# Kernel tuning notes

Measured on AMD Instinct MI355X. Metric: run time of the kernel, lower is better.

Reference implementation:

```python
import jax, jax.numpy as jnp
import numpy as np

# ---- constants from the module ----
E_L, E_e, E_i = -65.0, 0.0, -80.0
V_th, V_reset, V_floor = -50.0, -65.0, -200.0
dt = 0.25
T_STEPS = 4000
DECAY_AMPA = float(np.exp(-dt / 2.0))   # tau_ampa = 2.0
DECAY_GABA = float(np.exp(-dt / 9.0))   # tau_gaba = 9.0
C_M_E, G_L_E = 1.0, 1.0 / 20.0          # tau_m_E = 20
C_M_I, G_L_I = 0.5, 0.5 / 5.0           # tau_m_I = 5
REF_E = 12                               # round(3.0/0.25)
REF_I = 6                                # round(1.5/0.25)
CM_BACK = 80.0
SLOPE = 1.0                              # biophysical surrogate slope

@jax.custom_vjp
def spike(u):
    # Heaviside forward, fast-sigmoid surrogate backward (SurrogateSpike)
    return (u >= 0).astype(u.dtype)

def _spike_fwd(u):
    return (u >= 0).astype(u.dtype), u

def _spike_bwd(u, g):
    return (g * SLOPE / (1.0 + SLOPE * jnp.abs(u)) ** 2,)

spike.defvjp(_spike_fwd, _spike_bwd)

def _scale_grad(x, scale):
    # forward identity, gradient scaled by `scale`
    return x * scale + jax.lax.stop_gradient(x) * (1.0 - scale)

def lif_step(v, I_total, ref, C_m, g_L, ref_steps):
    dv = (dt / C_m) * (-g_L * (v - E_L) + I_total)
    dv = _scale_grad(dv, 1.0 / CM_BACK)
    v = jnp.maximum(v + dv, V_floor)
    ref = jnp.maximum(ref - 1, 0)
    can_spike = ref == 0
    s = spike(v - V_th) * can_spike.astype(v.dtype)
    spiked_or_ref = (s > 0) | ~can_spike
    v = jnp.where(spiked_or_ref, V_reset, v)
    ref = jnp.where(s > 0, ref_steps, ref)
    return v, s, ref

def setup_inputs() -> dict:
    key = jax.random.key(0)
    ks = jax.random.split(key, 6)
    T, B, N_IN, N_E, N_I, N_OUT = T_STEPS, 64, 64, 256, 64, 10

    def init_w(k, shape, mean, std):
        # init_weight: N(mean,std) clamped >=0, fan-in normalized
        w = jnp.maximum(jax.random.normal(k, shape, jnp.float32) * std + mean, 0.0)
        return w / shape[0]

    return {
        "input_spikes": (jax.random.uniform(ks[0], (T, B, N_IN)) < 0.02).astype(jnp.float32),
        "W_ff0": init_w(ks[1], (N_IN, N_E), 5.1, 3.8),
        "W_ff1": init_w(ks[2], (N_E, N_OUT), 5.1, 3.8),
        "W_ee": init_w(ks[3], (N_E, N_E), 0.0, 0.0),
        "W_ei": init_w(ks[4], (N_E, N_I), 1.0, 0.5),
        "W_ie": init_w(ks[5], (N_I, N_E), 3.0, 1.5),
    }

def reference(input_spikes, W_ff0, W_ff1, W_ee, W_ei, W_ie):
    # Dale's law: feedforward weights clamped >= 0 in forward
    W0 = jnp.maximum(W_ff0, 0.0)
    W1 = jnp.maximum(W_ff1, 0.0)
    B = input_spikes.shape[1]
    N_E, N_I, N_OUT = W0.shape[1], W_ei.shape[1], W1.shape[1]
    f32 = input_spikes.dtype

    z = lambda n: jnp.zeros((B, n), f32)
    vl = lambda n: jnp.full((B, n), E_L, f32)
    zr = lambda n: jnp.zeros((B, n), jnp.int32)

    carry0 = (vl(N_E), zr(N_E), z(N_E), z(N_E), z(N_E),   # E pop: v, ref, g_ampa, g_gaba, spikes
              vl(N_I), zr(N_I), z(N_I), z(N_I),           # I pop: v, ref, g_ampa, spikes
              vl(N_OUT), zr(N_OUT), z(N_OUT),             # out pop: v, ref, g_ampa
              z(N_OUT))                                    # output spike accumulator

    def step(c, s_in):
        v_e, r_e, ge_e, gi_e, s_e, v_i, r_i, ge_i, s_i, v_o, r_o, g_o, acc = c
        # exp_synapse: spike kicks first, then decay
        ge_e = (ge_e + s_in @ W0 + s_e @ W_ee) * DECAY_AMPA
        gi_e = (gi_e + s_i @ W_ie) * DECAY_GABA
        ge_i = (ge_i + s_e @ W_ei) * DECAY_AMPA
        # E neurons: COBA with excitation + inhibition
        v_e, s_e, r_e = lif_step(v_e, ge_e * (E_e - v_e) + gi_e * (E_i - v_e), r_e, C_M_E, G_L_E, REF_E)
        # I neurons: COBA excitation only
        v_i, s_i, r_i = lif_step(v_i, ge_i * (E_e - v_i), r_i, C_M_I, G_L_I, REF_I)
        # output layer driven by fresh E spikes
        g_o = (g_o + s_e @ W1) * DECAY_AMPA
        v_o, s_o, r_o = lif_step(v_o, g_o * (E_e - v_o), r_o, C_M_E, G_L_E, REF_E)
        acc = acc + s_o
        return (v_e, r_e, ge_e, gi_e, s_e, v_i, r_i, ge_i, s_i, v_o, r_o, g_o, acc), None

    cT, _ = jax.lax.scan(step, carry0, input_spikes)
    return cT[-1]  # [B, N_OUT] output spike counts over T_steps
```

## Files before the change

### kernel.cpp

```cpp
#include <hip/hip_runtime.h>
#include <math.h>

#pragma clang fp contract(off)

#define BB 64
#define N_IN 64
#define N_E 256
#define N_I 64
#define N_OUT 10

__device__ inline unsigned long long rfl64(unsigned long long x) {
  unsigned int lo = __builtin_amdgcn_readfirstlane((unsigned int)x);
  unsigned int hi = __builtin_amdgcn_readfirstlane((unsigned int)(x >> 32));
  return (((unsigned long long)hi) << 32) | (unsigned long long)lo;
}

__global__ __launch_bounds__(256, 1) void ping_kernel(
    const float* __restrict__ g_in,
    const float* __restrict__ g_W0,
    const float* __restrict__ g_W1,
    const float* __restrict__ g_Wee,
    const float* __restrict__ g_Wei,
    const float* __restrict__ g_Wie,
    float* __restrict__ g_out,
    int T, float dA, float dG)
{
  const int tid  = threadIdx.x;
  const int lane = tid & 63;
  const int wav  = tid >> 6;
  const int b    = blockIdx.x;
  const int col  = (lane < N_OUT) ? lane : 0;
  const int colO = 64 + col;

  __shared__ float sWie[N_I * N_E];
  __shared__ float sWeiO[N_E * 80];
  __shared__ float sZeroRow[256];
  __shared__ float sP[2][4][64];
  __shared__ float sKo[2][4][16];
  __shared__ __align__(16) unsigned sTag[2][4];
  __shared__ unsigned long long sME[2][4];
  __shared__ int sWee;

  {
    const float4* s0 = (const float4*)g_Wie; float4* d0 = (float4*)sWie;
    for (int k = tid; k < (N_I * N_E) / 4; k += 256) d0[k] = s0[k];
    {
      int j = tid;
      float* row = &sWeiO[j * 80];
      for (int c = 0; c < 64; ++c) row[c] = g_Wei[j * N_I + c];
      for (int o = 0; o < N_OUT; ++o) row[64 + o] = fmaxf(g_W1[j * N_OUT + o], 0.f);
      for (int c = 74; c < 80; ++c) row[c] = 0.f;
    }
  }
  sZeroRow[tid] = 0.f;
  if (tid < 4) { sME[0][tid] = 0ull; sME[1][tid] = 0ull; }
  if (tid < 8) sTag[tid >> 2][tid & 3] = 0u;
  if (tid == 0) sWee = 0;
  {
    bool any = false;
    const float4* p = (const float4*)g_Wee;
    for (int k = tid; k < (N_E * N_E) / 4; k += 256) {
      float4 x = p[k];
      any |= (x.x != 0.f) | (x.y != 0.f) | (x.z != 0.f) | (x.w != 0.f);
    }
    if (__ballot(any) != 0ull && lane == 0) sWee = 1;
  }
  __syncthreads();
  const int wee = sWee;

  float vE = -65.f, ge = 0.f, gi = 0.f; int rE = 0;
  float vI = -65.f, gI = 0.f; int rI = 0;
  float vO = -65.f, gO = 0.f, accO = 0.f; int rO = 0;

  unsigned long long mE = 0ull;
  unsigned long long mI = 0ull;

  float cur = g_in[b * N_IN + lane];
  float n1  = g_in[((T > 1 ? 1 : 0) * BB + b) * N_IN + lane];

  unsigned long long mInC = __ballot(cur != 0.f);
  unsigned long long aRemC = 0ull;
  bool vaC[4] = {false, false, false, false};
  float fwC[4];
  if (mInC) {
    unsigned long long a = mInC;
    int ja[4];
#pragma unroll
    for (int k = 0; k < 4; ++k) {
      vaC[k] = (a != 0ull); ja[k] = vaC[k] ? (__ffsll(a) - 1) : 0; a &= (a - 1ull);
    }
    aRemC = a;
#pragma unroll
    for (int k = 0; k < 4; ++k) fwC[k] = g_W0[ja[k] * N_E + tid];
  }

  const int base64 = wav * 64;

  if (!wee) {
    for (int t = 0; t < T; ++t) {
      const int slot = t & 1;
      const int tp = (t + 2 < T) ? (t + 2) : (T - 1);
      float n2 = g_in[(tp * BB + b) * N_IN + lane];

      float pEI = 0.f, kow = 0.f;
      {
        unsigned long long e = mE;
        while (e) {
          const float* qb[4];
#pragma unroll
          for (int k = 0; k < 4; ++k) {
            bool v = (e != 0ull); int j = v ? (__ffsll(e) - 1) : 0; e &= (e - 1ull);
            qb[k] = v ? &sWeiO[(base64 + j) * 80] : sZeroRow;
          }
          float fq[4], fr[4];
#pragma unroll
          for (int k = 0; k < 4; ++k) { fq[k] = qb[k][lane]; fr[k] = qb[k][colO]; }
#pragma unroll
          for (int k = 0; k < 4; ++k) pEI += fq[k];
#pragma unroll
          for (int k = 0; k < 4; ++k) kow += fr[k];
        }
      }

      sP[slot][wav][lane] = pEI;
      if (lane < 16) sKo[slot][wav][lane] = kow;
      asm volatile("s_waitcnt lgkmcnt(0)" ::: "memory");
      if (lane == 0) *((volatile unsigned*)&sTag[slot][wav]) = (unsigned)(t + 1);

      float kie = 0.f;
      {
        unsigned long long c = mI;
        while (c) {
          const float* pb[8];
#pragma unroll
          for (int k = 0; k < 8; ++k) {
            bool v = (c != 0ull); int j = v ? (__ffsll(c) - 1) : 0; c &= (c - 1ull);
            pb[k] = v ? &sWie[j * N_E] : sZeroRow;
          }
          float fI[8];
#pragma unroll
          for (int k = 0; k < 8; ++k) fI[k] = pb[k][tid];
#pragma unroll
          for (int k = 0; k < 8; ++k) kie += fI[k];
        }
      }

      float kin = 0.f;
      if (mInC) {
#pragma unroll
        for (int k = 0; k < 4; ++k) kin += vaC[k] ? fmaxf(fwC[k], 0.f) : 0.f;
        while (aRemC) {
          int j = __ffsll(aRemC) - 1; aRemC &= (aRemC - 1ull);
          kin += fmaxf(g_W0[j * N_E + tid], 0.f);
        }
      }

      ge = (ge + kin) * dA;
      gi = (gi + kie) * dG;
      {
        float t2 = ge * (0.f - vE);
        float t3 = gi * (-80.f - vE);
        float Itot = t2 + t3;
        float dv = 0.25f * ((-0.05f) * (vE - (-65.f)) + Itot);
        dv = dv * 0.0125f + dv * 0.9875f;
        vE = fmaxf(vE + dv, -200.f);
        rE = rE - 1; if (rE < 0) rE = 0;
        bool can = (rE == 0);
        bool sE = ((vE - (-50.f)) >= 0.f) && can;
        vE = (sE || !can) ? -65.f : vE;
        rE = sE ? 12 : rE;
        mE = __ballot(sE);
      }

      mInC = __ballot(n1 != 0.f);
      aRemC = 0ull;
      vaC[0] = vaC[1] = vaC[2] = vaC[3] = false;
      if (mInC) {
        unsigned long long a = mInC;
        int ja[4];
#pragma unroll
        for (int k = 0; k < 4; ++k) {
          vaC[k] = (a != 0ull); ja[k] = vaC[k] ? (__ffsll(a) - 1) : 0; a &= (a - 1ull);
        }
        aRemC = a;
#pragma unroll
        for (int k = 0; k < 4; ++k) fwC[k] = g_W0[ja[k] * N_E + tid];
      }

      {
        const unsigned want = (unsigned)(t + 1);
        const unsigned long long want2 = (((unsigned long long)want) << 32) | want;
        volatile unsigned long long* vt = (volatile unsigned long long*)&sTag[slot][0];
        while (true) {
          unsigned long long a0 = vt[0], a1 = vt[1];
          if (((a0 ^ want2) | (a1 ^ want2)) == 0ull) break;
        }
        asm volatile("" ::: "memory");
      }

      float p0 = sP[slot][0][lane], p1 = sP[slot][1][lane];
      float p2 = sP[slot][2][lane], p3 = sP[slot][3][lane];
      float k0 = sKo[slot][0][col], k1 = sKo[slot][1][col];
      float k2 = sKo[slot][2][col], k3 = sKo[slot][3][col];

      {
        float p = ((p0 + p1) + p2) + p3;
        gI = (gI + p) * dA;
        float Ii = gI * (0.f - vI);
        float dvi = 0.5f * ((-0.1f) * (vI - (-65.f)) + Ii);
        dvi = dvi * 0.0125f + dvi * 0.9875f;
        vI = fmaxf(vI + dvi, -200.f);
        rI = rI - 1; if (rI < 0) rI = 0;
        bool canI = (rI == 0);
        bool sI = ((vI - (-50.f)) >= 0.f) && canI;
        vI = (sI || !canI) ? -65.f : vI;
        rI = sI ? 6 : rI;
        mI = __ballot(sI);
      }

      {
        float ko = ((k0 + k1) + k2) + k3;
        gO = (gO + ko) * dA;
        float Io = gO * (0.f - vO);
        float dvo = 0.25f * ((-0.05f) * (vO - (-65.f)) + Io);
        dvo = dvo * 0.0125f + dvo * 0.9875f;
        vO = fmaxf(vO + dvo, -200.f);
        rO = rO - 1; if (rO < 0) rO = 0;
        bool canO = (rO == 0);
        bool sO = ((vO - (-50.f)) >= 0.f) && canO;
        vO = (sO || !canO) ? -65.f : vO;
        rO = sO ? 12 : rO;
        accO += sO ? 1.f : 0.f;
      }

      cur = n1; n1 = n2;
    }
  } else {
    unsigned long long we0 = 0ull, we1 = 0ull, we2 = 0ull, we3 = 0ull;
    for (int t = 0; t < T; ++t) {
      const int slot = t & 1;
      const int tp = (t + 2 < T) ? (t + 2) : (T - 1);
      float n2 = g_in[(tp * BB + b) * N_IN + lane];

      float pEI = 0.f, kow = 0.f;
      {
        unsigned long long e = mE;
        while (e) {
          const float* qb[4];
#pragma unroll
          for (int k = 0; k < 4; ++k) {
            bool v = (e != 0ull); int j = v ? (__ffsll(e) - 1) : 0; e &= (e - 1ull);
            qb[k] = v ? &sWeiO[(base64 + j) * 80] : sZeroRow;
          }
          float fq[4], fr[4];
#pragma unroll
          for (int k = 0; k < 4; ++k) { fq[k] = qb[k][lane]; fr[k] = qb[k][colO]; }
#pragma unroll
          for (int k = 0; k < 4; ++k) pEI += fq[k];
#pragma unroll
          for (int k = 0; k < 4; ++k) kow += fr[k];
        }
      }
      sP[slot][wav][lane] = pEI;
      if (lane < 16) sKo[slot][wav][lane] = kow;
      asm volatile("s_waitcnt lgkmcnt(0)" ::: "memory");
      if (lane == 0) *((volatile unsigned*)&sTag[slot][wav]) = (unsigned)(t + 1);

      float kie = 0.f;
      {
        unsigned long long c = mI;
        while (c) {
          const float* pb[8];
#pragma unroll
          for (int k = 0; k < 8; ++k) {
            bool v = (c != 0ull); int j = v ? (__ffsll(c) - 1) : 0; c &= (c - 1ull);
            pb[k] = v ? &sWie[j * N_E] : sZeroRow;
          }
          float fI[8];
#pragma unroll
          for (int k = 0; k < 8; ++k) fI[k] = pb[k][tid];
#pragma unroll
          for (int k = 0; k < 8; ++k) kie += fI[k];
        }
      }

      float kin = 0.f;
      if (mInC) {
#pragma unroll
        for (int k = 0; k < 4; ++k) kin += vaC[k] ? fmaxf(fwC[k], 0.f) : 0.f;
        while (aRemC) {
          int j = __ffsll(aRemC) - 1; aRemC &= (aRemC - 1ull);
          kin += fmaxf(g_W0[j * N_E + tid], 0.f);
        }
      }

      float kee = 0.f;
      {
        unsigned long long m0 = we0, m1 = we1, m2 = we2, m3 = we3;
        while (m0 | m1 | m2 | m3) {
          bool h0 = (m0 != 0ull), h1 = (m1 != 0ull), h2 = (m2 != 0ull), h3 = (m3 != 0ull);
          int idx = 0;
          if (h0)      { idx = __ffsll(m0) - 1;       m0 &= (m0 - 1ull); }
          else if (h1) { idx = 64 + __ffsll(m1) - 1;  m1 &= (m1 - 1ull); }
          else if (h2) { idx = 128 + __ffsll(m2) - 1; m2 &= (m2 - 1ull); }
          else if (h3) { idx = 192 + __ffsll(m3) - 1; m3 &= (m3 - 1ull); }
          kee += g_Wee[idx * N_E + tid];
        }
      }

      ge = ((ge + kin) + kee) * dA;
      gi = (gi + kie) * dG;
      {
        float t2 = ge * (0.f - vE);
        float t3 = gi * (-80.f - vE);
        float Itot = t2 + t3;
        float dv = 0.25f * ((-0.05f) * (vE - (-65.f)) + Itot);
        dv = dv * 0.0125f + dv * 0.9875f;
        vE = fmaxf(vE + dv, -200.f);
        rE = rE - 1; if (rE < 0) rE = 0;
        bool can = (rE == 0);
        bool sE = ((vE - (-50.f)) >= 0.f) && can;
        vE = (sE || !can) ? -65.f : vE;
        rE = sE ? 12 : rE;
        unsigned long long fresh = __ballot(sE);
        if (lane == 0) sME[slot][wav] = fresh;
        mE = fresh;
      }

      mInC = __ballot(n1 != 0.f);
      aRemC = 0ull;
      vaC[0] = vaC[1] = vaC[2] = vaC[3] = false;
      if (mInC) {
        unsigned long long a = mInC;
        int ja[4];
#pragma unroll
        for (int k = 0; k < 4; ++k) {
          vaC[k] = (a != 0ull); ja[k] = vaC[k] ? (__ffsll(a) - 1) : 0; a &= (a - 1ull);
        }
        aRemC = a;
#pragma unroll
        for (int k = 0; k < 4; ++k) fwC[k] = g_W0[ja[k] * N_E + tid];
      }

      {
        const unsigned want = (unsigned)(t + 1);
        const unsigned long long want2 = (((unsigned long long)want) << 32) | want;
        volatile unsigned long long* vt = (volatile unsigned long long*)&sTag[slot][0];
        while (true) {
          unsigned long long a0 = vt[0], a1 = vt[1];
          if (((a0 ^ want2) | (a1 ^ want2)) == 0ull) break;
        }
        asm volatile("" ::: "memory");
      }

      float p0 = sP[slot][0][lane], p1 = sP[slot][1][lane];
      float p2 = sP[slot][2][lane], p3 = sP[slot][3][lane];
      float k0 = sKo[slot][0][col], k1 = sKo[slot][1][col];
      float k2 = sKo[slot][2][col], k3 = sKo[slot][3][col];

      {
        float p = ((p0 + p1) + p2) + p3;
        gI = (gI + p) * dA;
        float Ii = gI * (0.f - vI);
        float dvi = 0.5f * ((-0.1f) * (vI - (-65.f)) + Ii);
        dvi = dvi * 0.0125f + dvi * 0.9875f;
        vI = fmaxf(vI + dvi, -200.f);
        rI = rI - 1; if (rI < 0) rI = 0;
        bool canI = (rI == 0);
        bool sI = ((vI - (-50.f)) >= 0.f) && canI;
        vI = (sI || !canI) ? -65.f : vI;
        rI = sI ? 6 : rI;
        mI = __ballot(sI);
      }

      {
        float ko = ((k0 + k1) + k2) + k3;
        gO = (gO + ko) * dA;
        float Io = gO * (0.f - vO);
        float dvo = 0.25f * ((-0.05f) * (vO - (-65.f)) + Io);
        dvo = dvo * 0.0125f + dvo * 0.9875f;
        vO = fmaxf(vO + dvo, -200.f);
        rO = rO - 1; if (rO < 0) rO = 0;
        bool canO = (rO == 0);
        bool sO = ((vO - (-50.f)) >= 0.f) && canO;
        vO = (sO || !canO) ? -65.f : vO;
        rO = sO ? 12 : rO;
        accO += sO ? 1.f : 0.f;
      }

      __syncthreads();
      we0 = rfl64(sME[slot][0]); we1 = rfl64(sME[slot][1]);
      we2 = rfl64(sME[slot][2]); we3 = rfl64(sME[slot][3]);

      cur = n1; n1 = n2;
    }
  }

  {
    float kd = 0.f;
    unsigned long long e = mE;
    while (e) {
      const float* rb[4];
#pragma unroll
      for (int k = 0; k < 4; ++k) {
        bool v = (e != 0ull); int j = v ? (__ffsll(e) - 1) : 0; e &= (e - 1ull);
        rb[k] = v ? &sWeiO[(base64 + j) * 80] : sZeroRow;
      }
      float fr[4];
#pragma unroll
      for (int k = 0; k < 4; ++k) fr[k] = rb[k][colO];
#pragma unroll
      for (int k = 0; k < 4; ++k) kd += fr[k];
    }
    __syncthreads();
    sP[0][wav][lane] = kd;
    __syncthreads();
    float ko = ((sP[0][0][col] + sP[0][1][col]) + sP[0][2][col]) + sP[0][3][col];
    gO = (gO + ko) * dA;
    float Io = gO * (0.f - vO);
    float dvo = 0.25f * ((-0.05f) * (vO - (-65.f)) + Io);
    dvo = dvo * 0.0125f + dvo * 0.9875f;
    vO = fmaxf(vO + dvo, -200.f);
    rO = rO - 1; if (rO < 0) rO = 0;
    bool canO = (rO == 0);
    bool sO = ((vO - (-50.f)) >= 0.f) && canO;
    accO += sO ? 1.f : 0.f;
  }

  if (wav == 0 && lane < N_OUT) g_out[b * N_OUT + lane] = accO;
}

extern "C" void kernel_launch(void* const* d_in, const int* in_sizes, int n_in,
                              void* d_out, int out_size, void* d_ws, size_t ws_size,
                              hipStream_t stream) {
  const float* g_in  = (const float*)d_in[0];
  const float* g_W0  = (const float*)d_in[1];
  const float* g_W1  = (const float*)d_in[2];
  const float* g_Wee = (const float*)d_in[3];
  const float* g_Wei = (const float*)d_in[4];
  const float* g_Wie = (const float*)d_in[5];
  float* out = (float*)d_out;
  int T = in_sizes[0] / (BB * N_IN);
  float dA = (float)exp(-0.25 / 2.0);
  float dG = (float)exp(-0.25 / 9.0);
  ping_kernel<<<dim3(BB), dim3(256), 0, stream>>>(g_in, g_W0, g_W1, g_Wee, g_Wei, g_Wie, out, T, dA, dG);
}
```

Measured before the change: 4.891 ms.

## Prefetch inhibitory weight rows early and relax tag-barrier waits

Right after the I-population spike mask is computed, the kernel now issues the LDS loads of the first eight W_ie rows for the next step's inhibitory current, so their latency overlaps the remaining work. It also drops the explicit lgkmcnt wait before publishing the per-wave tag, relying on in-order LDS writes within a wave. It reads the tags once early so the spin loop can be skipped when all waves have already arrived. These changes target LDS latency and barrier stall on the serial time-step critical path, at the cost of extra live registers and a reliance on LDS ordering for correctness.

Result: no change. 4.937 ms (+0.9%).

```diff
diff --git a/kernel.cpp b/kernel.cpp
--- a/kernel.cpp
+++ b/kernel.cpp
@@ -75,6 +75,10 @@
   unsigned long long mE = 0ull;
   unsigned long long mI = 0ull;
 
+  float kieF[8];
+  unsigned long long kieRem = 0ull;
+  unsigned long long mIPrev = 0ull;
+
   float cur = g_in[b * N_IN + lane];
   float n1  = g_in[((T > 1 ? 1 : 0) * BB + b) * N_IN + lane];
 
@@ -124,17 +128,21 @@
 
       sP[slot][wav][lane] = pEI;
       if (lane < 16) sKo[slot][wav][lane] = kow;
-      asm volatile("s_waitcnt lgkmcnt(0)" ::: "memory");
+      asm volatile("" ::: "memory");
       if (lane == 0) *((volatile unsigned*)&sTag[slot][wav]) = (unsigned)(t + 1);
 
+      unsigned long long pr0 = ((volatile unsigned long long*)&sTag[slot][0])[0];
+      unsigned long long pr1 = ((volatile unsigned long long*)&sTag[slot][0])[1];
+
       float kie = 0.f;
-      {
-        unsigned long long c = mI;
-        while (c) {
+      if (mIPrev) {
+#pragma unroll
+        for (int k = 0; k < 8; ++k) kie += kieF[k];
+        while (kieRem) {
           const float* pb[8];
 #pragma unroll
           for (int k = 0; k < 8; ++k) {
-            bool v = (c != 0ull); int j = v ? (__ffsll(c) - 1) : 0; c &= (c - 1ull);
+            bool v = (kieRem != 0ull); int j = v ? (__ffsll(kieRem) - 1) : 0; kieRem &= (kieRem - 1ull);
             pb[k] = v ? &sWie[j * N_E] : sZeroRow;
           }
           float fI[8];
@@ -190,10 +198,12 @@
       {
         const unsigned want = (unsigned)(t + 1);
         const unsigned long long want2 = (((unsigned long long)want) << 32) | want;
-        volatile unsigned long long* vt = (volatile unsigned long long*)&sTag[slot][0];
-        while (true) {
-          unsigned long long a0 = vt[0], a1 = vt[1];
-          if (((a0 ^ want2) | (a1 ^ want2)) == 0ull) break;
+        if ((((pr0 ^ want2) | (pr1 ^ want2))) != 0ull) {
+          volatile unsigned long long* vt = (volatile unsigned long long*)&sTag[slot][0];
+          while (true) {
+            unsigned long long a0 = vt[0], a1 = vt[1];
+            if (((a0 ^ want2) | (a1 ^ want2)) == 0ull) break;
+          }
         }
         asm volatile("" ::: "memory");
       }
@@ -216,6 +226,20 @@
         vI = (sI || !canI) ? -65.f : vI;
         rI = sI ? 6 : rI;
         mI = __ballot(sI);
+      }
+
+      mIPrev = mI;
+      if (mI) {
+        unsigned long long c = mI;
+        const float* pb[8];
+#pragma unroll
+        for (int k = 0; k < 8; ++k) {
+          bool v = (c != 0ull); int j = v ? (__ffsll(c) - 1) : 0; c &= (c - 1ull);
+          pb[k] = v ? &sWie[j * N_E] : sZeroRow;
+        }
+        kieRem = c;
+#pragma unroll
+        for (int k = 0; k < 8; ++k) kieF[k] = pb[k][tid];
       }
 
       {
@@ -413,9 +437,11 @@
       for (int k = 0; k < 4; ++k) kd += fr[k];
     }
     __syncthreads();
-    sP[0][wav][lane] = kd;
+    if (lane < 16) sKo[0][wav][lane] = kd;
     __syncthreads();
-    float ko = ((sP[0][0][col] + sP[0][1][col]) + sP[0][2][col]) + sP[0][3][col];
+    float k0 = sKo[0][0][col], k1 = sKo[0][1][col];
+    float k2 = sKo[0][2][col], k3 = sKo[0][3][col];
+    float ko = ((k0 + k1) + k2) + k3;
     gO = (gO + ko) * dA;
     float Io = gO * (0.f - vO);
     float dvo = 0.25f * ((-0.05f) * (vO - (-65.f)) + Io);
```
